# Kernel optimization log

Measured on AMD Instinct MI355X. Metric: run time of the kernel, lower is better.

Reference implementation:

```python
import jax, jax.numpy as jnp
import numpy as np
from jax import lax

B, C, H, W = 256, 7, 128, 128   # batch, num_bands, img_size, img_size
HID = 256                        # scorer hidden width
SEL = 3                          # selected_bands


def setup_inputs() -> dict:
    key = jax.random.key(0)
    k = jax.random.split(key, 7)
    n = H * W
    x = jax.random.normal(k[0], (B, C, H, W), dtype=jnp.float32)
    # to_qkv: Linear(num_bands, 3*num_bands); stored (in, out) for x @ w. Dead code
    # in the original forward (attn_output unused) but kept for parameter parity.
    w_qkv = jax.random.normal(k[1], (C, 3 * C), dtype=jnp.float32) * (1.0 / np.sqrt(C))
    b_qkv = jnp.zeros((3 * C,), dtype=jnp.float32)
    # band_score_proj: Linear(n, 256) -> ReLU -> Linear(256, 1)
    w1 = jax.random.normal(k[2], (n, HID), dtype=jnp.float32) * (1.0 / np.sqrt(n))
    b1 = jax.random.normal(k[3], (HID,), dtype=jnp.float32) * 0.01
    w2 = jax.random.normal(k[4], (HID, 1), dtype=jnp.float32) * (1.0 / np.sqrt(HID))
    b2 = jax.random.normal(k[5], (1,), dtype=jnp.float32) * 0.01
    return {"x": x, "w_qkv": w_qkv, "b_qkv": b_qkv, "w1": w1, "b1": b1, "w2": w2, "b2": b2}


def reference(x, w_qkv, b_qkv, w1, b1, w2, b2):
    b, c, h, w = x.shape
    feat = x.reshape(b, c, h * w)                  # b c n  (== x_flat.transpose(1,2))
    # NOTE: the original also runs a 1-dim-per-head SDPA on x_flat whose result
    # (attn_output) is never used in the returned values; it is omitted here.
    hid = jax.nn.relu(jnp.einsum('bcn,nk->bck', feat, w1) + b1)   # b c 256
    band_scores = (jnp.einsum('bck,ko->bco', hid, w2) + b2)[..., 0]  # b c
    _, top_indices = lax.top_k(band_scores, SEL)                  # b sel
    selected = jnp.take_along_axis(x, top_indices[:, :, None, None], axis=1)  # b sel h w
    return selected, top_indices
```

## Files before the change

### kernel.cpp

```cpp
#include <hip/hip_runtime.h>

#define Bn    256
#define Cc    7
#define Nn    16384
#define HIDW  256
#define SEL   3
#define Mrows (Bn * Cc)
#define KSPLIT 16
#define KCHUNK (Nn / KSPLIT)
#define BK    32
#define PART_STRIDE ((size_t)Mrows * HIDW)

typedef __attribute__((ext_vector_type(8))) short bf16x8;
typedef __attribute__((ext_vector_type(4))) float floatx4;

__device__ __forceinline__ unsigned short bf16_rne(float f) {
    unsigned int u = __float_as_uint(f);
    unsigned int r = u + 0x7fffu + ((u >> 16) & 1u);
    return (unsigned short)(r >> 16);
}

__device__ __forceinline__ uint4 pack8(const unsigned short* p) {
    uint4 v;
    v.x = (unsigned)p[0] | ((unsigned)p[1] << 16);
    v.y = (unsigned)p[2] | ((unsigned)p[3] << 16);
    v.z = (unsigned)p[4] | ((unsigned)p[5] << 16);
    v.w = (unsigned)p[6] | ((unsigned)p[7] << 16);
    return v;
}

__global__ __launch_bounds__(256) void convert_w1(const float* __restrict__ w1,
                                                  unsigned short* __restrict__ bhi,
                                                  unsigned short* __restrict__ blo) {
    const int id = blockIdx.x * 256 + threadIdx.x;
    const int l  = id & 63;
    const int ct = id >> 6;
    const int T  = ct & 15;
    const int c  = ct >> 4;
    const int n  = T * 16 + (l & 15);
    const int k  = c * 32 + (l >> 4) * 8;
    unsigned short hi[8], lo[8];
#pragma unroll
    for (int j = 0; j < 8; ++j) {
        float f = w1[(size_t)(k + j) * HIDW + n];
        unsigned short h = bf16_rne(f);
        float fh = __uint_as_float((unsigned)h << 16);
        hi[j] = h;
        lo[j] = bf16_rne(f - fh);
    }
    *(uint4*)(bhi + (size_t)id * 8) = pack8(hi);
    *(uint4*)(blo + (size_t)id * 8) = pack8(lo);
}

__global__ __launch_bounds__(256) void gemm_mfma(const float* __restrict__ A,
                                                 const unsigned short* __restrict__ Bhi,
                                                 const unsigned short* __restrict__ Blo,
                                                 float* __restrict__ part) {
    __shared__ unsigned short Ah[4096], Al[4096], Bh[4096], Bl[4096];

    const int bx = blockIdx.x;
    const int m0 = blockIdx.y * 128;
    const int s  = blockIdx.z;
    const int k0 = s * KCHUNK;
    const int t  = threadIdx.x;
    const int lane = t & 63;
    const int w    = t >> 6;
    const int wm   = w & 1;
    const int wn   = w >> 1;

    const int ar  = t >> 1;
    const int kof = (t & 1) * 16;
    const float* aptr = A + (size_t)(m0 + ar) * Nn + k0 + kof;
    const int aidx0 = (ar >> 4) * 512 + ((ar & 15) + ((kof >> 3) + 0) * 16) * 8;
    const int aidx1 = (ar >> 4) * 512 + ((ar & 15) + ((kof >> 3) + 1) * 16) * 8;

    floatx4 acc[4][4];
#pragma unroll
    for (int i = 0; i < 4; ++i)
#pragma unroll
        for (int j = 0; j < 4; ++j) acc[i][j] = (floatx4)0.0f;

    for (int kk = 0; kk < KCHUNK; kk += BK) {
        float4 a0 = *(const float4*)(aptr + kk + 0);
        float4 a1 = *(const float4*)(aptr + kk + 4);
        float4 a2 = *(const float4*)(aptr + kk + 8);
        float4 a3 = *(const float4*)(aptr + kk + 12);
        const size_t bbase = ((size_t)(((k0 + kk) >> 5) * 16 + bx * 8)) * 512;
        uint4 bh0 = *(const uint4*)(Bhi + bbase + t * 8);
        uint4 bh1 = *(const uint4*)(Bhi + bbase + 2048 + t * 8);
        uint4 bl0 = *(const uint4*)(Blo + bbase + t * 8);
        uint4 bl1 = *(const uint4*)(Blo + bbase + 2048 + t * 8);

        float af[16] = {a0.x, a0.y, a0.z, a0.w, a1.x, a1.y, a1.z, a1.w,
                        a2.x, a2.y, a2.z, a2.w, a3.x, a3.y, a3.z, a3.w};
        unsigned short hi[16], lo[16];
#pragma unroll
        for (int j = 0; j < 16; ++j) {
            unsigned short h = bf16_rne(af[j]);
            hi[j] = h;
            lo[j] = bf16_rne(af[j] - __uint_as_float((unsigned)h << 16));
        }

        __syncthreads();
        *(uint4*)&Ah[aidx0] = pack8(hi);
        *(uint4*)&Ah[aidx1] = pack8(hi + 8);
        *(uint4*)&Al[aidx0] = pack8(lo);
        *(uint4*)&Al[aidx1] = pack8(lo + 8);
        *(uint4*)&Bh[t * 8]        = bh0;
        *(uint4*)&Bh[2048 + t * 8] = bh1;
        *(uint4*)&Bl[t * 8]        = bl0;
        *(uint4*)&Bl[2048 + t * 8] = bl1;
        __syncthreads();

        bf16x8 fah[4], fal[4], fbh[4], fbl[4];
#pragma unroll
        for (int i = 0; i < 4; ++i) {
            fah[i] = *(const bf16x8*)&Ah[(wm * 4 + i) * 512 + lane * 8];
            fal[i] = *(const bf16x8*)&Al[(wm * 4 + i) * 512 + lane * 8];
        }
#pragma unroll
        for (int j = 0; j < 4; ++j) {
            fbh[j] = *(const bf16x8*)&Bh[(wn * 4 + j) * 512 + lane * 8];
            fbl[j] = *(const bf16x8*)&Bl[(wn * 4 + j) * 512 + lane * 8];
        }
#pragma unroll
        for (int i = 0; i < 4; ++i)
#pragma unroll
            for (int j = 0; j < 4; ++j) {
                acc[i][j] = __builtin_amdgcn_mfma_f32_16x16x32_bf16(fah[i], fbh[j], acc[i][j], 0, 0, 0);
                acc[i][j] = __builtin_amdgcn_mfma_f32_16x16x32_bf16(fah[i], fbl[j], acc[i][j], 0, 0, 0);
                acc[i][j] = __builtin_amdgcn_mfma_f32_16x16x32_bf16(fal[i], fbh[j], acc[i][j], 0, 0, 0);
            }
    }

    const int row4 = (lane >> 4) * 4;
    const int col  = lane & 15;
    float* base = part + (size_t)s * PART_STRIDE;
#pragma unroll
    for (int i = 0; i < 4; ++i)
#pragma unroll
        for (int j = 0; j < 4; ++j) {
            const int n = bx * 128 + wn * 64 + j * 16 + col;
#pragma unroll
            for (int p = 0; p < 4; ++p) {
                const int m = m0 + wm * 64 + i * 16 + row4 + p;
                base[(size_t)m * HIDW + n] = acc[i][j][p];
            }
        }
}

__global__ __launch_bounds__(256) void score_topk(const float* __restrict__ part,
                                                  const float* __restrict__ b1,
                                                  const float* __restrict__ w2,
                                                  const float* __restrict__ b2,
                                                  float* __restrict__ out,
                                                  int* __restrict__ sidx) {
    const int b = blockIdx.x;
    const int t = threadIdx.x;
    __shared__ float red[4];
    __shared__ float sc[Cc];
    const float bias = b1[t];
    const float wv   = w2[t];

    for (int c = 0; c < Cc; ++c) {
        const size_t row = (size_t)(b * Cc + c) * HIDW + t;
        float h = 0.0f;
#pragma unroll
        for (int s2 = 0; s2 < KSPLIT; ++s2) h += part[(size_t)s2 * PART_STRIDE + row];
        float p = fmaxf(h + bias, 0.0f) * wv;
#pragma unroll
        for (int off = 32; off > 0; off >>= 1) p += __shfl_down(p, off, 64);
        if ((t & 63) == 0) red[t >> 6] = p;
        __syncthreads();
        if (t == 0) sc[c] = red[0] + red[1] + red[2] + red[3] + b2[0];
        __syncthreads();
    }

    if (t == 0) {
        bool used[Cc] = {};
#pragma unroll
        for (int k = 0; k < SEL; ++k) {
            int best = 0;
            float bv = -3.4e38f;
#pragma unroll
            for (int c = 0; c < Cc; ++c)
                if (!used[c] && sc[c] > bv) { bv = sc[c]; best = c; }
            used[best] = true;
            sidx[b * SEL + k] = best;
            out[(size_t)Bn * SEL * Nn + b * SEL + k] = (float)best;
        }
    }
}

__global__ __launch_bounds__(256) void gather_bands(const float* __restrict__ x,
                                                    const int* __restrict__ sidx,
                                                    float* __restrict__ out) {
    const int id = blockIdx.x;
    const int b  = id / SEL;
    const int band = sidx[id];
    const float4* src = (const float4*)(x + (size_t)(b * Cc + band) * Nn);
    float4* dst = (float4*)(out + (size_t)id * Nn);
    for (int i = threadIdx.x; i < Nn / 4; i += 256) dst[i] = src[i];
}

extern "C" void kernel_launch(void* const* d_in, const int* in_sizes, int n_in,
                              void* d_out, int out_size, void* d_ws, size_t ws_size,
                              hipStream_t stream) {
    const float* x  = (const float*)d_in[0];
    const float* w1 = (const float*)d_in[3];
    const float* b1 = (const float*)d_in[4];
    const float* w2 = (const float*)d_in[5];
    const float* b2 = (const float*)d_in[6];
    float* out = (float*)d_out;

    char* ws = (char*)d_ws;
    float* part = (float*)ws;
    unsigned short* bhi = (unsigned short*)(ws + KSPLIT * PART_STRIDE * sizeof(float));
    unsigned short* blo = bhi + (size_t)Nn * HIDW;
    int* sidx = (int*)(blo + (size_t)Nn * HIDW);

    convert_w1<<<(Nn / 32) * 16 * 64 / 256, 256, 0, stream>>>(w1, bhi, blo);
    gemm_mfma<<<dim3(HIDW / 128, Mrows / 128, KSPLIT), 256, 0, stream>>>(x, bhi, blo, part);
    score_topk<<<Bn, 256, 0, stream>>>(part, b1, w2, b2, out, sidx);
    gather_bands<<<Bn * SEL, 256, 0, stream>>>(x, sidx, out);
}
```

Measured before the change: 266.1 us.

## Truncate-split bf16, load B tiles directly to LDS, split scoring and top-k

Replaces round-to-nearest bf16 hi/lo splitting with mask truncation plus byte-permute packing, which cuts ALU work in the conversion and GEMM staging. B tiles are loaded global-to-LDS directly when the builtin is available, so they no longer pass through registers. The score/top-k kernel is split into a per-row scoring kernel with 1792 blocks and a single-block top-k kernel, and the b2 bias is dropped because it does not change the ranking. Truncation gives a slightly different hi/lo split, but hi+lo still captures the value closely. The extra launch adds some overhead.

```diff
diff --git a/kernel.cpp b/kernel.cpp
--- a/kernel.cpp
+++ b/kernel.cpp
@@ -14,19 +14,25 @@
 typedef __attribute__((ext_vector_type(8))) short bf16x8;
 typedef __attribute__((ext_vector_type(4))) float floatx4;
 
-__device__ __forceinline__ unsigned short bf16_rne(float f) {
-    unsigned int u = __float_as_uint(f);
-    unsigned int r = u + 0x7fffu + ((u >> 16) & 1u);
-    return (unsigned short)(r >> 16);
-}
-
-__device__ __forceinline__ uint4 pack8(const unsigned short* p) {
-    uint4 v;
-    v.x = (unsigned)p[0] | ((unsigned)p[1] << 16);
-    v.y = (unsigned)p[2] | ((unsigned)p[3] << 16);
-    v.z = (unsigned)p[4] | ((unsigned)p[5] << 16);
-    v.w = (unsigned)p[6] | ((unsigned)p[7] << 16);
-    return v;
+#if __has_builtin(__builtin_amdgcn_global_load_lds)
+#define HAS_GLDS 1
+#endif
+
+__device__ __forceinline__ unsigned pack_hi16(unsigned ua, unsigned ub) {
+#if __has_builtin(__builtin_amdgcn_perm)
+    return __builtin_amdgcn_perm(ub, ua, 0x07060302u);
+#else
+    return (ua >> 16) | (ub & 0xffff0000u);
+#endif
+}
+
+__device__ __forceinline__ void split2(float a, float b, unsigned& hp, unsigned& lp) {
+    unsigned ua = __float_as_uint(a), ub = __float_as_uint(b);
+    float fa = __uint_as_float(ua & 0xffff0000u);
+    float fb = __uint_as_float(ub & 0xffff0000u);
+    float la = a - fa, lb = b - fb;
+    hp = pack_hi16(ua, ub);
+    lp = pack_hi16(__float_as_uint(la), __float_as_uint(lb));
 }
 
 __global__ __launch_bounds__(256) void convert_w1(const float* __restrict__ w1,
@@ -39,17 +45,14 @@
     const int c  = ct >> 4;
     const int n  = T * 16 + (l & 15);
     const int k  = c * 32 + (l >> 4) * 8;
-    unsigned short hi[8], lo[8];
-#pragma unroll
-    for (int j = 0; j < 8; ++j) {
-        float f = w1[(size_t)(k + j) * HIDW + n];
-        unsigned short h = bf16_rne(f);
-        float fh = __uint_as_float((unsigned)h << 16);
-        hi[j] = h;
-        lo[j] = bf16_rne(f - fh);
-    }
-    *(uint4*)(bhi + (size_t)id * 8) = pack8(hi);
-    *(uint4*)(blo + (size_t)id * 8) = pack8(lo);
+    float f[8];
+#pragma unroll
+    for (int j = 0; j < 8; ++j) f[j] = w1[(size_t)(k + j) * HIDW + n];
+    unsigned hp[4], lp[4];
+#pragma unroll
+    for (int m = 0; m < 4; ++m) split2(f[2 * m], f[2 * m + 1], hp[m], lp[m]);
+    *(uint4*)(bhi + (size_t)id * 8) = make_uint4(hp[0], hp[1], hp[2], hp[3]);
+    *(uint4*)(blo + (size_t)id * 8) = make_uint4(lp[0], lp[1], lp[2], lp[3]);
 }
 
 __global__ __launch_bounds__(256) void gemm_mfma(const float* __restrict__ A,
@@ -73,6 +76,7 @@
     const float* aptr = A + (size_t)(m0 + ar) * Nn + k0 + kof;
     const int aidx0 = (ar >> 4) * 512 + ((ar & 15) + ((kof >> 3) + 0) * 16) * 8;
     const int aidx1 = (ar >> 4) * 512 + ((ar & 15) + ((kof >> 3) + 1) * 16) * 8;
+    const int wbase = (t & 192) * 8;
 
     floatx4 acc[4][4];
 #pragma unroll
@@ -86,30 +90,43 @@
         float4 a2 = *(const float4*)(aptr + kk + 8);
         float4 a3 = *(const float4*)(aptr + kk + 12);
         const size_t bbase = ((size_t)(((k0 + kk) >> 5) * 16 + bx * 8)) * 512;
+
+#ifndef HAS_GLDS
         uint4 bh0 = *(const uint4*)(Bhi + bbase + t * 8);
         uint4 bh1 = *(const uint4*)(Bhi + bbase + 2048 + t * 8);
         uint4 bl0 = *(const uint4*)(Blo + bbase + t * 8);
         uint4 bl1 = *(const uint4*)(Blo + bbase + 2048 + t * 8);
-
+#endif
         float af[16] = {a0.x, a0.y, a0.z, a0.w, a1.x, a1.y, a1.z, a1.w,
                         a2.x, a2.y, a2.z, a2.w, a3.x, a3.y, a3.z, a3.w};
-        unsigned short hi[16], lo[16];
-#pragma unroll
-        for (int j = 0; j < 16; ++j) {
-            unsigned short h = bf16_rne(af[j]);
-            hi[j] = h;
-            lo[j] = bf16_rne(af[j] - __uint_as_float((unsigned)h << 16));
-        }
+        unsigned hp[8], lp[8];
+#pragma unroll
+        for (int m = 0; m < 8; ++m) split2(af[2 * m], af[2 * m + 1], hp[m], lp[m]);
 
         __syncthreads();
-        *(uint4*)&Ah[aidx0] = pack8(hi);
-        *(uint4*)&Ah[aidx1] = pack8(hi + 8);
-        *(uint4*)&Al[aidx0] = pack8(lo);
-        *(uint4*)&Al[aidx1] = pack8(lo + 8);
+#ifdef HAS_GLDS
+        __builtin_amdgcn_global_load_lds(
+            (const __attribute__((address_space(1))) void*)(Bhi + bbase + t * 8),
+            (__attribute__((address_space(3))) void*)&Bh[wbase], 16, 0, 0);
+        __builtin_amdgcn_global_load_lds(
+            (const __attribute__((address_space(1))) void*)(Bhi + bbase + 2048 + t * 8),
+            (__attribute__((address_space(3))) void*)&Bh[2048 + wbase], 16, 0, 0);
+        __builtin_amdgcn_global_load_lds(
+            (const __attribute__((address_space(1))) void*)(Blo + bbase + t * 8),
+            (__attribute__((address_space(3))) void*)&Bl[wbase], 16, 0, 0);
+        __builtin_amdgcn_global_load_lds(
+            (const __attribute__((address_space(1))) void*)(Blo + bbase + 2048 + t * 8),
+            (__attribute__((address_space(3))) void*)&Bl[2048 + wbase], 16, 0, 0);
+#else
         *(uint4*)&Bh[t * 8]        = bh0;
         *(uint4*)&Bh[2048 + t * 8] = bh1;
         *(uint4*)&Bl[t * 8]        = bl0;
         *(uint4*)&Bl[2048 + t * 8] = bl1;
+#endif
+        *(uint4*)&Ah[aidx0] = make_uint4(hp[0], hp[1], hp[2], hp[3]);
+        *(uint4*)&Ah[aidx1] = make_uint4(hp[4], hp[5], hp[6], hp[7]);
+        *(uint4*)&Al[aidx0] = make_uint4(lp[0], lp[1], lp[2], lp[3]);
+        *(uint4*)&Al[aidx1] = make_uint4(lp[4], lp[5], lp[6], lp[7]);
         __syncthreads();
 
         bf16x8 fah[4], fal[4], fbh[4], fbl[4];
@@ -149,46 +166,43 @@
         }
 }
 
-__global__ __launch_bounds__(256) void score_topk(const float* __restrict__ part,
+__global__ __launch_bounds__(256) void score_rows(const float* __restrict__ part,
                                                   const float* __restrict__ b1,
                                                   const float* __restrict__ w2,
-                                                  const float* __restrict__ b2,
-                                                  float* __restrict__ out,
-                                                  int* __restrict__ sidx) {
-    const int b = blockIdx.x;
+                                                  float* __restrict__ scores) {
+    const int r = blockIdx.x;
     const int t = threadIdx.x;
+    const size_t off = (size_t)r * HIDW + t;
+    float h = 0.0f;
+#pragma unroll
+    for (int s = 0; s < KSPLIT; ++s) h += part[(size_t)s * PART_STRIDE + off];
+    float p = fmaxf(h + b1[t], 0.0f) * w2[t];
+#pragma unroll
+    for (int o = 32; o > 0; o >>= 1) p += __shfl_down(p, o, 64);
     __shared__ float red[4];
-    __shared__ float sc[Cc];
-    const float bias = b1[t];
-    const float wv   = w2[t];
-
-    for (int c = 0; c < Cc; ++c) {
-        const size_t row = (size_t)(b * Cc + c) * HIDW + t;
-        float h = 0.0f;
-#pragma unroll
-        for (int s2 = 0; s2 < KSPLIT; ++s2) h += part[(size_t)s2 * PART_STRIDE + row];
-        float p = fmaxf(h + bias, 0.0f) * wv;
-#pragma unroll
-        for (int off = 32; off > 0; off >>= 1) p += __shfl_down(p, off, 64);
-        if ((t & 63) == 0) red[t >> 6] = p;
-        __syncthreads();
-        if (t == 0) sc[c] = red[0] + red[1] + red[2] + red[3] + b2[0];
-        __syncthreads();
-    }
-
-    if (t == 0) {
-        bool used[Cc] = {};
-#pragma unroll
-        for (int k = 0; k < SEL; ++k) {
-            int best = 0;
-            float bv = -3.4e38f;
-#pragma unroll
-            for (int c = 0; c < Cc; ++c)
-                if (!used[c] && sc[c] > bv) { bv = sc[c]; best = c; }
-            used[best] = true;
-            sidx[b * SEL + k] = best;
-            out[(size_t)Bn * SEL * Nn + b * SEL + k] = (float)best;
-        }
+    if ((t & 63) == 0) red[t >> 6] = p;
+    __syncthreads();
+    if (t == 0) scores[r] = red[0] + red[1] + red[2] + red[3];
+}
+
+__global__ __launch_bounds__(256) void topk_kernel(const float* __restrict__ scores,
+                                                   float* __restrict__ out,
+                                                   int* __restrict__ sidx) {
+    const int b = threadIdx.x;
+    float sc[Cc];
+#pragma unroll
+    for (int c = 0; c < Cc; ++c) sc[c] = scores[b * Cc + c];
+    bool used[Cc] = {};
+#pragma unroll
+    for (int k = 0; k < SEL; ++k) {
+        int best = 0;
+        float bv = -3.4e38f;
+#pragma unroll
+        for (int c = 0; c < Cc; ++c)
+            if (!used[c] && sc[c] > bv) { bv = sc[c]; best = c; }
+        used[best] = true;
+        sidx[b * SEL + k] = best;
+        out[(size_t)Bn * SEL * Nn + b * SEL + k] = (float)best;
     }
 }
 
@@ -211,16 +225,19 @@
     const float* b1 = (const float*)d_in[4];
     const float* w2 = (const float*)d_in[5];
     const float* b2 = (const float*)d_in[6];
+    (void)b2;
     float* out = (float*)d_out;
 
     char* ws = (char*)d_ws;
     float* part = (float*)ws;
     unsigned short* bhi = (unsigned short*)(ws + KSPLIT * PART_STRIDE * sizeof(float));
     unsigned short* blo = bhi + (size_t)Nn * HIDW;
-    int* sidx = (int*)(blo + (size_t)Nn * HIDW);
+    int*   sidx   = (int*)(blo + (size_t)Nn * HIDW);
+    float* scores = (float*)(sidx + Bn * SEL);
 
     convert_w1<<<(Nn / 32) * 16 * 64 / 256, 256, 0, stream>>>(w1, bhi, blo);
     gemm_mfma<<<dim3(HIDW / 128, Mrows / 128, KSPLIT), 256, 0, stream>>>(x, bhi, blo, part);
-    score_topk<<<Bn, 256, 0, stream>>>(part, b1, w2, b2, out, sidx);
+    score_rows<<<Mrows, 256, 0, stream>>>(part, b1, w2, scores);
+    topk_kernel<<<1, 256, 0, stream>>>(scores, out, sidx);
     gather_bands<<<Bn * SEL, 256, 0, stream>>>(x, sidx, out);
 }
```

Result: no change. 263.5 us (-1.0%).
